# Kernel tuning notes

Measured on AMD Instinct MI355X. Metric: run time of the kernel, lower is better.

The kernel has to match this reference:

```python
import jax, jax.numpy as jnp
import numpy as np

NUM_HEADS = 16
HEAD_DIM = 64  # hidden_size / num_heads


def setup_inputs() -> dict:
    key = jax.random.key(0)
    ks = jax.random.split(key, 20)
    B, S, H, K = 16, 1024, 1024, 64
    d = {"hidden_states": jax.random.normal(ks[0], (B, S, H), jnp.float32)}
    i = 1
    for p in ("q", "k", "v", "o"):
        d["W" + p] = jax.random.normal(ks[i], (H, H), jnp.float32) * (1.0 / np.sqrt(H)); i += 1
        d["b" + p] = jax.random.normal(ks[i], (H,), jnp.float32) * 0.02; i += 1
        d["LM" + p] = jax.random.normal(ks[i], (H, K), jnp.float32) * (1.0 / np.sqrt(K)); i += 1
        d["RM" + p] = jax.random.normal(ks[i], (K, H), jnp.float32) * (1.0 / np.sqrt(H)); i += 1
        d["F" + p] = jnp.ones((H,), jnp.float32)
    d["task"] = 0
    return d


def _proj(x, W, b, LM, RM, F):
    # RG weight reconstruction: weight = LM @ RM + W  (task==0 branch)
    w = LM @ RM + W  # [h_out, h_in]
    y = jnp.einsum("bsi,oi->bso", x, w) + b
    return y * F  # SFG per-channel scaling


def reference(hidden_states, Wq, bq, LMq, RMq, Fq, Wk, bk, LMk, RMk, Fk,
              Wv, bv, LMv, RMv, Fv, Wo, bo, LMo, RMo, Fo, task):
    B, S, H = hidden_states.shape
    nh, hd = NUM_HEADS, HEAD_DIM
    q = _proj(hidden_states, Wq, bq, LMq, RMq, Fq).reshape(B, S, nh, hd)
    k = _proj(hidden_states, Wk, bk, LMk, RMk, Fk).reshape(B, S, nh, hd)
    v = _proj(hidden_states, Wv, bv, LMv, RMv, Fv).reshape(B, S, nh, hd)
    scores = jnp.einsum("bqhd,bkhd->bhqk", q, k) / np.sqrt(hd).astype(np.float32)
    probs = jax.nn.softmax(scores, axis=-1)  # attn_dropout rate = 0.0
    ctx = jnp.einsum("bhqk,bkhd->bqhd", probs, v).reshape(B, S, H)
    out = _proj(ctx, Wo, bo, LMo, RMo, Fo)  # proj_dropout rate = 0.0
    return out
```

## Files before the change

kernel.cpp:

```cpp
#include <hip/hip_runtime.h>
#include <cstdint>
#include <cstddef>

typedef short short8 __attribute__((ext_vector_type(8)));
typedef float f32x4 __attribute__((ext_vector_type(4)));
typedef float f32x16 __attribute__((ext_vector_type(16)));
typedef unsigned short us4 __attribute__((ext_vector_type(4)));

__device__ __forceinline__ unsigned short f2bf(float f) {
  unsigned int u = __float_as_uint(f);
  unsigned int r = (u + 0x7fffu + ((u >> 16) & 1u)) >> 16;
  return (unsigned short)r;
}
__device__ __forceinline__ float exp2_fast(float x) {
  return __builtin_amdgcn_exp2f(x);
}
__device__ __forceinline__ unsigned int cvt_pk_bf16(float a, float b) {
  unsigned int d;
  asm("v_cvt_pk_bf16_f32 %0, %1, %2" : "=v"(d) : "v"(a), "v"(b));
  return d;
}
__device__ __forceinline__ void permlane32_swap2(unsigned int& a, unsigned int& b) {
  asm("v_permlane32_swap_b32 %0, %1" : "+v"(a), "+v"(b));
}
__device__ __forceinline__ void gload_lds16(const void* g, void* l) {
  auto gp = reinterpret_cast<const __attribute__((address_space(1))) char*>(
      reinterpret_cast<uintptr_t>(g));
  auto lp = reinterpret_cast<__attribute__((address_space(3))) char*>(
      reinterpret_cast<uintptr_t>(l));
  __builtin_amdgcn_global_load_lds(gp, lp, 16, 0, 0);
}

__global__ __launch_bounds__(256) void prep_weights(
    const float* __restrict__ W, const float* __restrict__ bias,
    const float* __restrict__ LM, const float* __restrict__ RM,
    const float* __restrict__ F, float scale,
    unsigned short* __restrict__ Wout, float* __restrict__ bout) {
  const int o = blockIdx.x;
  const int tid = threadIdx.x;
  __shared__ float lm[64];
  if (tid < 64) lm[tid] = LM[o * 64 + tid];
  __syncthreads();
  const float f = F[o] * scale;
#pragma unroll
  for (int j = 0; j < 4; ++j) {
    const int i = tid + j * 256;
    float acc = W[o * 1024 + i];
#pragma unroll 16
    for (int k = 0; k < 64; ++k) acc = fmaf(lm[k], RM[k * 1024 + i], acc);
    Wout[o * 1024 + i] = f2bf(acc * f);
  }
  if (tid == 0) bout[o] = bias[o] * f;
}

__global__ __launch_bounds__(256) void cast_x(const float* __restrict__ x,
                                              unsigned short* __restrict__ y, int n4) {
  const int i = blockIdx.x * 256 + threadIdx.x;
  if (i >= n4) return;
  f32x4 v = *(const f32x4*)(x + (size_t)i * 4);
  us4 o;
  o[0] = f2bf(v[0]); o[1] = f2bf(v[1]); o[2] = f2bf(v[2]); o[3] = f2bf(v[3]);
  *(us4*)(y + (size_t)i * 4) = o;
}

template <int MODE>
__global__ __launch_bounds__(256) void gemm_bt(const unsigned short* __restrict__ A,
                                               const unsigned short* __restrict__ Bw,
                                               const float* __restrict__ bias,
                                               void* __restrict__ Cout,
                                               int M, int N, int K) {
  __shared__ unsigned short sA[128 * 64];
  __shared__ unsigned short sB[128 * 64];
  const int tid = threadIdx.x;
  const int w = tid >> 6;
  const int lane = tid & 63;
  const int quad = lane >> 4;
  const int ln = lane & 15;
  const int bm = blockIdx.x, bn = blockIdx.y;
  const int wm = w >> 1, wn = w & 1;

  f32x4 acc[4][4];
#pragma unroll
  for (int a = 0; a < 4; ++a)
#pragma unroll
    for (int b = 0; b < 4; ++b) acc[a][b] = (f32x4){0.f, 0.f, 0.f, 0.f};

  const size_t Kb = (size_t)K * 2;
  const char* Agb = (const char*)A + (size_t)bm * 128 * Kb;
  const char* Bgb = (const char*)Bw + (size_t)bn * 128 * Kb;
  char* sAb = (char*)sA;
  char* sBb = (char*)sB;
  const int sw = ln & 7;

  for (int k0 = 0; k0 < K; k0 += 64) {
    __syncthreads();
#pragma unroll
    for (int i = 0; i < 4; ++i) {
      const int Lb = w * 4096 + i * 1024 + lane * 16;
      const int r = Lb >> 7;
      const int c = (Lb >> 4) & 7;
      const int cb = ((c ^ (r & 7)) * 16);
      gload_lds16(Agb + (size_t)r * Kb + (size_t)k0 * 2 + cb, sAb + Lb);
      gload_lds16(Bgb + (size_t)r * Kb + (size_t)k0 * 2 + cb, sBb + Lb);
    }
    __syncthreads();
#pragma unroll
    for (int kk = 0; kk < 2; ++kk) {
      short8 af[4], bfv[4];
#pragma unroll
      for (int t = 0; t < 4; ++t) {
        const int ch = ((kk * 4 + quad) ^ sw) * 16;
        af[t]  = *(const short8*)(sAb + (wm * 64 + t * 16 + ln) * 128 + ch);
        bfv[t] = *(const short8*)(sBb + (wn * 64 + t * 16 + ln) * 128 + ch);
      }
#pragma unroll
      for (int mt = 0; mt < 4; ++mt)
#pragma unroll
        for (int nt = 0; nt < 4; ++nt)
          acc[mt][nt] = __builtin_amdgcn_mfma_f32_16x16x32_bf16(af[mt], bfv[nt], acc[mt][nt], 0, 0, 0);
    }
  }

  if (MODE == 0) {
    unsigned short* out = (unsigned short*)Cout;
#pragma unroll
    for (int mt = 0; mt < 4; ++mt) {
#pragma unroll
      for (int nt = 0; nt < 4; ++nt) {
        const int gn = bn * 128 + wn * 64 + nt * 16 + ln;
        const float bv = bias[gn];
        const int pidx = gn >> 10, rem = gn & 1023;
        const int hh = rem >> 6, dd = rem & 63;
        const int gm0 = bm * 128 + wm * 64 + mt * 16 + quad * 4;
        const int bb = gm0 >> 10, ss0 = gm0 & 1023;
        if (pidx < 2) {
#pragma unroll
          for (int r = 0; r < 4; ++r) {
            const size_t off = ((((size_t)pidx * 16 + bb) * 16 + hh) * 1024 + (ss0 + r)) * 64 + dd;
            out[off] = f2bf(acc[mt][nt][r] + bv);
          }
        } else {
          us4 pk;
#pragma unroll
          for (int r = 0; r < 4; ++r) pk[r] = f2bf(acc[mt][nt][r] + bv);
          const size_t off = (size_t)2 * 16777216 +
                             (((size_t)(bb * 16 + hh) * 64 + dd) * 1024 + ss0);
          *(us4*)(out + off) = pk;
        }
      }
    }
  } else {
    float* out = (float*)Cout;
#pragma unroll
    for (int mt = 0; mt < 4; ++mt) {
#pragma unroll
      for (int nt = 0; nt < 4; ++nt) {
        const int gn = bn * 128 + wn * 64 + nt * 16 + ln;
        const float bv = bias[gn];
#pragma unroll
        for (int r = 0; r < 4; ++r) {
          const int gm = bm * 128 + wm * 64 + mt * 16 + quad * 4 + r;
          out[(size_t)gm * N + gn] = acc[mt][nt][r] + bv;
        }
      }
    }
  }
}

__global__ __launch_bounds__(256) void attn(const unsigned short* __restrict__ Qb,
                                            const unsigned short* __restrict__ Kb_,
                                            const unsigned short* __restrict__ VTb,
                                            unsigned short* __restrict__ ctx) {
  __shared__ unsigned short sK[2][64 * 64];
  __shared__ unsigned short sVT[2][64 * 64];
  const int tid = threadIdx.x;
  const int w = tid >> 6, lane = tid & 63;
  const int col = lane & 31, hi = lane >> 5;
  const int sw7 = col & 7;
  const int bid = blockIdx.x;
  const int xcd = bid & 7, qt = (bid >> 3) & 7, sbh = bid >> 6;
  const int bh = xcd * 32 + sbh;
  const int b = bh >> 4, h = bh & 15;

  short8 bq[4];
  {
    const unsigned short* Qg =
        Qb + ((size_t)bh * 1024 + (size_t)qt * 128 + w * 32 + col) * 64 + hi * 8;
#pragma unroll
    for (int ks = 0; ks < 4; ++ks) bq[ks] = *(const short8*)(Qg + ks * 16);
  }

  f32x16 accO[2];
#pragma unroll
  for (int nt = 0; nt < 2; ++nt)
#pragma unroll
    for (int r = 0; r < 16; ++r) accO[nt][r] = 0.f;
  float mrun = -3e38f, lrun = 0.f;

  const char* Kbase = (const char*)Kb_ + (size_t)bh * 131072;
  const char* Vbase = (const char*)VTb + (size_t)bh * 131072;

  auto stage = [&](int kt, int buf) {
#pragma unroll
    for (int i = 0; i < 2; ++i) {
      const int Lb = w * 2048 + i * 1024 + lane * 16;
      const int r = Lb >> 7;
      const int c = (Lb >> 4) & 7;
      const int cb = ((c ^ (r & 7)) * 16);
      gload_lds16(Kbase + (size_t)kt * 8192 + (size_t)r * 128 + cb, (char*)sK[buf] + Lb);
      gload_lds16(Vbase + (size_t)kt * 128 + (size_t)r * 2048 + cb, (char*)sVT[buf] + Lb);
    }
  };

  stage(0, 0);

  for (int kt = 0; kt < 16; ++kt) {
    const int cur = kt & 1;
    const char* sKb = (const char*)sK[cur];
    const char* sVb = (const char*)sVT[cur];

    stage((kt + 1) & 15, cur ^ 1);
    asm volatile("s_waitcnt vmcnt(4)" ::: "memory");
    __builtin_amdgcn_s_barrier();
    asm volatile("" ::: "memory");

    f32x16 accS[2];
#pragma unroll
    for (int mt = 0; mt < 2; ++mt)
#pragma unroll
      for (int r = 0; r < 16; ++r) accS[mt][r] = 0.f;
#pragma unroll
    for (int ks = 0; ks < 4; ++ks) {
      const int ch = (((2 * ks + hi) ^ sw7) * 16);
      const short8 ak0 = *(const short8*)(sKb + (col)*128 + ch);
      const short8 ak1 = *(const short8*)(sKb + (32 + col) * 128 + ch);
      __builtin_amdgcn_s_setprio(1);
      accS[0] = __builtin_amdgcn_mfma_f32_32x32x16_bf16(ak0, bq[ks], accS[0], 0, 0, 0);
      accS[1] = __builtin_amdgcn_mfma_f32_32x32x16_bf16(ak1, bq[ks], accS[1], 0, 0, 0);
      __builtin_amdgcn_s_setprio(0);
    }

    float tmax = -3e38f;
#pragma unroll
    for (int mt = 0; mt < 2; ++mt)
#pragma unroll
      for (int r = 0; r < 16; ++r) tmax = fmaxf(tmax, accS[mt][r]);
    tmax = fmaxf(tmax, __shfl_xor(tmax, 32));
    if (!__all(tmax <= mrun + 8.0f)) {
      const float mnew = fmaxf(mrun, tmax);
      const float alpha = exp2_fast(mrun - mnew);
      mrun = mnew;
      lrun *= alpha;
#pragma unroll
      for (int r = 0; r < 16; ++r) {
        const float ar = __shfl(alpha, (r & 3) + 8 * (r >> 2) + 4 * hi);
        accO[0][r] *= ar;
        accO[1][r] *= ar;
      }
    }
    const float m = mrun;

    float psum = 0.f;
#pragma unroll
    for (int mt = 0; mt < 2; ++mt) {
#pragma unroll
      for (int c = 0; c < 2; ++c) {
        const int r0 = c * 8;
        const float e0 = exp2_fast(accS[mt][r0 + 0] - m);
        const float e1 = exp2_fast(accS[mt][r0 + 1] - m);
        const float e2 = exp2_fast(accS[mt][r0 + 2] - m);
        const float e3 = exp2_fast(accS[mt][r0 + 3] - m);
        const float e4 = exp2_fast(accS[mt][r0 + 4] - m);
        const float e5 = exp2_fast(accS[mt][r0 + 5] - m);
        const float e6 = exp2_fast(accS[mt][r0 + 6] - m);
        const float e7 = exp2_fast(accS[mt][r0 + 7] - m);
        psum += ((e0 + e1) + (e2 + e3)) + ((e4 + e5) + (e6 + e7));
        unsigned int x = cvt_pk_bf16(e0, e1);
        unsigned int y = cvt_pk_bf16(e2, e3);
        unsigned int z = cvt_pk_bf16(e4, e5);
        unsigned int t = cvt_pk_bf16(e6, e7);
        permlane32_swap2(x, z);
        permlane32_swap2(y, t);
        union { unsigned int u[4]; short8 v; } pa;
        pa.u[0] = x; pa.u[1] = y; pa.u[2] = z; pa.u[3] = t;
        const int cs = mt * 4 + c * 2 + hi;
        const int ch = ((cs ^ sw7) * 16);
        const short8 bv0 = *(const short8*)(sVb + (col)*128 + ch);
        const short8 bv1 = *(const short8*)(sVb + (32 + col) * 128 + ch);
        __builtin_amdgcn_s_setprio(1);
        accO[0] = __builtin_amdgcn_mfma_f32_32x32x16_bf16(pa.v, bv0, accO[0], 0, 0, 0);
        accO[1] = __builtin_amdgcn_mfma_f32_32x32x16_bf16(pa.v, bv1, accO[1], 0, 0, 0);
        __builtin_amdgcn_s_setprio(0);
      }
    }
    lrun += psum;

    __builtin_amdgcn_s_barrier();
    asm volatile("" ::: "memory");
  }

  float lt = lrun + __shfl_xor(lrun, 32);
  const float inv = 1.0f / lt;
#pragma unroll
  for (int r = 0; r < 16; ++r) {
    const int qr = (r & 3) + 8 * (r >> 2) + 4 * hi;
    const float iv = __shfl(inv, qr);
    const int sg = qt * 128 + w * 32 + qr;
    const size_t base = ((size_t)(b * 1024 + sg)) * 1024 + h * 64;
    ctx[base + col] = f2bf(accO[0][r] * iv);
    ctx[base + 32 + col] = f2bf(accO[1][r] * iv);
  }
}

extern "C" void kernel_launch(void* const* d_in, const int* in_sizes, int n_in,
                              void* d_out, int out_size, void* d_ws, size_t ws_size,
                              hipStream_t stream) {
  const float* hs  = (const float*)d_in[0];
  const float* Wq  = (const float*)d_in[1];
  const float* bq  = (const float*)d_in[2];
  const float* LMq = (const float*)d_in[3];
  const float* RMq = (const float*)d_in[4];
  const float* Fq  = (const float*)d_in[5];
  const float* Wk  = (const float*)d_in[6];
  const float* bk  = (const float*)d_in[7];
  const float* LMk = (const float*)d_in[8];
  const float* RMk = (const float*)d_in[9];
  const float* Fk  = (const float*)d_in[10];
  const float* Wv  = (const float*)d_in[11];
  const float* bv  = (const float*)d_in[12];
  const float* LMv = (const float*)d_in[13];
  const float* RMv = (const float*)d_in[14];
  const float* Fv  = (const float*)d_in[15];
  const float* Wo  = (const float*)d_in[16];
  const float* bo  = (const float*)d_in[17];
  const float* LMo = (const float*)d_in[18];
  const float* RMo = (const float*)d_in[19];
  const float* Fo  = (const float*)d_in[20];

  char* p = (char*)d_ws;
  unsigned short* xbf  = (unsigned short*)p; p += (size_t)16384 * 1024 * 2;
  unsigned short* Wqkv = (unsigned short*)p; p += (size_t)3072 * 1024 * 2;
  unsigned short* Wob  = (unsigned short*)p; p += (size_t)1024 * 1024 * 2;
  float* bqkv = (float*)p; p += 3072 * 4;
  float* bob  = (float*)p; p += 1024 * 4;
  unsigned short* qkv = (unsigned short*)p; p += (size_t)3 * 16777216 * 2;
  unsigned short* ctx = (unsigned short*)p; p += (size_t)16777216 * 2;

  const float qscale = 0.125f * 1.4426950408889634f;

  cast_x<<<16384, 256, 0, stream>>>(hs, xbf, 16777216 / 4);
  prep_weights<<<1024, 256, 0, stream>>>(Wq, bq, LMq, RMq, Fq, qscale, Wqkv, bqkv);
  prep_weights<<<1024, 256, 0, stream>>>(Wk, bk, LMk, RMk, Fk, 1.0f, Wqkv + 1024 * 1024, bqkv + 1024);
  prep_weights<<<1024, 256, 0, stream>>>(Wv, bv, LMv, RMv, Fv, 1.0f, Wqkv + 2 * 1024 * 1024, bqkv + 2048);
  prep_weights<<<1024, 256, 0, stream>>>(Wo, bo, LMo, RMo, Fo, 1.0f, Wob, bob);

  gemm_bt<0><<<dim3(128, 24), 256, 0, stream>>>(xbf, Wqkv, bqkv, (void*)qkv, 16384, 3072, 1024);

  attn<<<2048, 256, 0, stream>>>(qkv, qkv + 16777216, qkv + 2 * 16777216, ctx);

  gemm_bt<1><<<dim3(128, 8), 256, 0, stream>>>(ctx, Wob, bob, d_out, 16384, 1024, 1024);
}
```

Measured before the change: 487.8 us.

## Double-buffer GEMM LDS tiles, remap blocks across XCDs, raise MFMA priority

The projection GEMM now double-buffers its A/B LDS tiles, issuing the next K-slice's global-to-LDS loads before computing on the current one, with a single barrier per iteration instead of two. Blocks are launched on a 1D grid and remapped so that consecutive tile IDs land on the same XCD, which should improve L2 reuse of the shared A rows. The MFMA burst is wrapped in s_setprio to favour issue of the math instructions. LDS use doubles to 64 KB per block, which may lower occupancy.

```diff
diff --git a/kernel.cpp b/kernel.cpp
--- a/kernel.cpp
+++ b/kernel.cpp
@@ -69,14 +69,17 @@
                                                const float* __restrict__ bias,
                                                void* __restrict__ Cout,
                                                int M, int N, int K) {
-  __shared__ unsigned short sA[128 * 64];
-  __shared__ unsigned short sB[128 * 64];
+  __shared__ unsigned short sA[2][128 * 64];
+  __shared__ unsigned short sB[2][128 * 64];
   const int tid = threadIdx.x;
   const int w = tid >> 6;
   const int lane = tid & 63;
   const int quad = lane >> 4;
   const int ln = lane & 15;
-  const int bm = blockIdx.x, bn = blockIdx.y;
+  const int nbn = N >> 7;
+  const int cpx = (int)gridDim.x >> 3;
+  const int wgid = ((int)blockIdx.x & 7) * cpx + ((int)blockIdx.x >> 3);
+  const int bm = wgid / nbn, bn = wgid - bm * nbn;
   const int wm = w >> 1, wn = w & 1;
 
   f32x4 acc[4][4];
@@ -88,36 +91,50 @@
   const size_t Kb = (size_t)K * 2;
   const char* Agb = (const char*)A + (size_t)bm * 128 * Kb;
   const char* Bgb = (const char*)Bw + (size_t)bn * 128 * Kb;
-  char* sAb = (char*)sA;
-  char* sBb = (char*)sB;
   const int sw = ln & 7;
-
-  for (int k0 = 0; k0 < K; k0 += 64) {
-    __syncthreads();
+  const int nt = K >> 6;
+
+  auto stage = [&](int k0, int buf) {
+    char* sAd = (char*)sA + buf * 16384;
+    char* sBd = (char*)sB + buf * 16384;
 #pragma unroll
     for (int i = 0; i < 4; ++i) {
       const int Lb = w * 4096 + i * 1024 + lane * 16;
       const int r = Lb >> 7;
       const int c = (Lb >> 4) & 7;
       const int cb = ((c ^ (r & 7)) * 16);
-      gload_lds16(Agb + (size_t)r * Kb + (size_t)k0 * 2 + cb, sAb + Lb);
-      gload_lds16(Bgb + (size_t)r * Kb + (size_t)k0 * 2 + cb, sBb + Lb);
-    }
-    __syncthreads();
+      gload_lds16(Agb + (size_t)r * Kb + (size_t)k0 * 2 + cb, sAd + Lb);
+      gload_lds16(Bgb + (size_t)r * Kb + (size_t)k0 * 2 + cb, sBd + Lb);
+    }
+  };
+
+  stage(0, 0);
+
+  for (int t = 0; t < nt; ++t) {
+    const int cur = t & 1;
+    asm volatile("s_waitcnt vmcnt(0)" ::: "memory");
+    __builtin_amdgcn_s_barrier();
+    asm volatile("" ::: "memory");
+    if (t + 1 < nt) stage((t + 1) << 6, cur ^ 1);
+
+    const char* sAc = (const char*)sA + cur * 16384;
+    const char* sBc = (const char*)sB + cur * 16384;
 #pragma unroll
     for (int kk = 0; kk < 2; ++kk) {
       short8 af[4], bfv[4];
 #pragma unroll
-      for (int t = 0; t < 4; ++t) {
+      for (int t4 = 0; t4 < 4; ++t4) {
         const int ch = ((kk * 4 + quad) ^ sw) * 16;
-        af[t]  = *(const short8*)(sAb + (wm * 64 + t * 16 + ln) * 128 + ch);
-        bfv[t] = *(const short8*)(sBb + (wn * 64 + t * 16 + ln) * 128 + ch);
-      }
+        af[t4]  = *(const short8*)(sAc + (wm * 64 + t4 * 16 + ln) * 128 + ch);
+        bfv[t4] = *(const short8*)(sBc + (wn * 64 + t4 * 16 + ln) * 128 + ch);
+      }
+      __builtin_amdgcn_s_setprio(1);
 #pragma unroll
       for (int mt = 0; mt < 4; ++mt)
 #pragma unroll
-        for (int nt = 0; nt < 4; ++nt)
-          acc[mt][nt] = __builtin_amdgcn_mfma_f32_16x16x32_bf16(af[mt], bfv[nt], acc[mt][nt], 0, 0, 0);
+        for (int ntc = 0; ntc < 4; ++ntc)
+          acc[mt][ntc] = __builtin_amdgcn_mfma_f32_16x16x32_bf16(af[mt], bfv[ntc], acc[mt][ntc], 0, 0, 0);
+      __builtin_amdgcn_s_setprio(0);
     }
   }
 
@@ -126,8 +143,8 @@
 #pragma unroll
     for (int mt = 0; mt < 4; ++mt) {
 #pragma unroll
-      for (int nt = 0; nt < 4; ++nt) {
-        const int gn = bn * 128 + wn * 64 + nt * 16 + ln;
+      for (int ntc = 0; ntc < 4; ++ntc) {
+        const int gn = bn * 128 + wn * 64 + ntc * 16 + ln;
         const float bv = bias[gn];
         const int pidx = gn >> 10, rem = gn & 1023;
         const int hh = rem >> 6, dd = rem & 63;
@@ -137,12 +154,12 @@
 #pragma unroll
           for (int r = 0; r < 4; ++r) {
             const size_t off = ((((size_t)pidx * 16 + bb) * 16 + hh) * 1024 + (ss0 + r)) * 64 + dd;
-            out[off] = f2bf(acc[mt][nt][r] + bv);
+            out[off] = f2bf(acc[mt][ntc][r] + bv);
           }
         } else {
           us4 pk;
 #pragma unroll
-          for (int r = 0; r < 4; ++r) pk[r] = f2bf(acc[mt][nt][r] + bv);
+          for (int r = 0; r < 4; ++r) pk[r] = f2bf(acc[mt][ntc][r] + bv);
           const size_t off = (size_t)2 * 16777216 +
                              (((size_t)(bb * 16 + hh) * 64 + dd) * 1024 + ss0);
           *(us4*)(out + off) = pk;
@@ -154,13 +171,13 @@
 #pragma unroll
     for (int mt = 0; mt < 4; ++mt) {
 #pragma unroll
-      for (int nt = 0; nt < 4; ++nt) {
-        const int gn = bn * 128 + wn * 64 + nt * 16 + ln;
+      for (int ntc = 0; ntc < 4; ++ntc) {
+        const int gn = bn * 128 + wn * 64 + ntc * 16 + ln;
         const float bv = bias[gn];
 #pragma unroll
         for (int r = 0; r < 4; ++r) {
           const int gm = bm * 128 + wm * 64 + mt * 16 + quad * 4 + r;
-          out[(size_t)gm * N + gn] = acc[mt][nt][r] + bv;
+          out[(size_t)gm * N + gn] = acc[mt][ntc][r] + bv;
         }
       }
     }
@@ -354,9 +371,9 @@
   prep_weights<<<1024, 256, 0, stream>>>(Wv, bv, LMv, RMv, Fv, 1.0f, Wqkv + 2 * 1024 * 1024, bqkv + 2048);
   prep_weights<<<1024, 256, 0, stream>>>(Wo, bo, LMo, RMo, Fo, 1.0f, Wob, bob);
 
-  gemm_bt<0><<<dim3(128, 24), 256, 0, stream>>>(xbf, Wqkv, bqkv, (void*)qkv, 16384, 3072, 1024);
+  gemm_bt<0><<<3072, 256, 0, stream>>>(xbf, Wqkv, bqkv, (void*)qkv, 16384, 3072, 1024);
 
   attn<<<2048, 256, 0, stream>>>(qkv, qkv + 16777216, qkv + 2 * 16777216, ctx);
 
-  gemm_bt<1><<<dim3(128, 8), 256, 0, stream>>>(ctx, Wob, bob, d_out, 16384, 1024, 1024);
-}
+  gemm_bt<1><<<1024, 256, 0, stream>>>(ctx, Wob, bob, d_out, 16384, 1024, 1024);
+}
```

New measurement: 506.8 us. +3.9%, slower.
